# Kernel optimization log

Hardware: AMD Instinct MI355X
Metric: run time of the kernel (lower is better)

Reference implementation:

```python
import jax, jax.numpy as jnp
import numpy as np
import math

D_MODEL = 2048
NUM_HEADS = 16
D_FF = 8192
HEAD_DIM = D_MODEL // NUM_HEADS
EPS = 1e-5


def _xavier(key, out_f, in_f):
    std = math.sqrt(2.0 / (in_f + out_f))
    return jax.random.normal(key, (out_f, in_f), dtype=jnp.float32) * std


def setup_inputs() -> dict:
    key = jax.random.key(0)
    ks = jax.random.split(key, 8)
    x = jax.random.normal(ks[0], (2, 2048, D_MODEL), dtype=jnp.float32)
    return {
        "x": x,
        "Wq": _xavier(ks[1], D_MODEL, D_MODEL),
        "Wk": _xavier(ks[2], D_MODEL, D_MODEL),
        "Wv": _xavier(ks[3], D_MODEL, D_MODEL),
        "Wo": _xavier(ks[4], D_MODEL, D_MODEL),
        "W1": _xavier(ks[5], D_FF, D_MODEL),
        "W2": _xavier(ks[6], D_MODEL, D_FF),
        "g1": jnp.ones((D_MODEL,), jnp.float32),
        "b1": jnp.zeros((D_MODEL,), jnp.float32),
        "g2": jnp.ones((D_MODEL,), jnp.float32),
        "b2": jnp.zeros((D_MODEL,), jnp.float32),
    }


def _ternary(w):
    # per-tensor abs-mean threshold -> {-1, 0, 1}
    abs_w = jnp.abs(w)
    thr = jnp.mean(abs_w)
    return jnp.where(abs_w > thr, jnp.sign(w), jnp.zeros_like(w))


def _tlin(x, w):
    # F.linear with ternarized weight [out, in], no bias
    return jnp.einsum("bsi,oi->bso", x, _ternary(w))


def _layernorm(x, g, b):
    mu = jnp.mean(x, axis=-1, keepdims=True)
    var = jnp.mean(jnp.square(x - mu), axis=-1, keepdims=True)
    return (x - mu) * jax.lax.rsqrt(var + EPS) * g + b


def reference(x, Wq, Wk, Wv, Wo, W1, W2, g1, b1, g2, b2):
    B, S, D = x.shape
    H, Hd = NUM_HEADS, HEAD_DIM
    q = _tlin(x, Wq).reshape(B, S, H, Hd).transpose(0, 2, 1, 3)  # bhsd
    k = _tlin(x, Wk).reshape(B, S, H, Hd).transpose(0, 2, 1, 3)
    v = _tlin(x, Wv).reshape(B, S, H, Hd).transpose(0, 2, 1, 3)
    scores = jnp.einsum("bhqd,bhkd->bhqk", q, k) / math.sqrt(Hd)
    probs = jax.nn.softmax(scores, axis=-1)
    attn = jnp.einsum("bhqk,bhkd->bhqd", probs, v)
    attn = attn.transpose(0, 2, 1, 3).reshape(B, S, D)
    attn = _tlin(attn, Wo)
    x = _layernorm(x + attn, g1, b1)  # dropout is identity in eval
    ff = _tlin(jax.nn.relu(_tlin(x, W1)), W2)
    x = _layernorm(x + ff, g2, b2)
    return x
```

## Files before the change

### kernel.cpp

```cpp
#include <hip/hip_runtime.h>
#include <hip/hip_bf16.h>

typedef __bf16 bf16_t;
typedef __bf16 bf16x8 __attribute__((ext_vector_type(8)));
typedef __bf16 bf16x4 __attribute__((ext_vector_type(4)));
typedef float f32x4 __attribute__((ext_vector_type(4)));
typedef int i32x4 __attribute__((ext_vector_type(4)));

__device__ __forceinline__ f32x4 mfma16(bf16x8 a, bf16x8 b, f32x4 c) {
  return __builtin_amdgcn_mfma_f32_16x16x32_bf16(a, b, c, 0, 0, 0);
}

__device__ __forceinline__ void gload16(const void* g, void* l) {
  __builtin_amdgcn_global_load_lds(
      (const __attribute__((address_space(1))) void*)g,
      (__attribute__((address_space(3))) void*)l, 16, 0, 0);
}

__global__ void abssum_all(const float* __restrict__ W0, const float* __restrict__ W1_,
                           const float* __restrict__ W2_, const float* __restrict__ W3,
                           const float* __restrict__ W4, const float* __restrict__ W5,
                           double* __restrict__ partial) {
  __shared__ double sd[256];
  const int w = blockIdx.y, tid = threadIdx.x;
  const float* W = (w == 0) ? W0 : (w == 1) ? W1_ : (w == 2) ? W2_ : (w == 3) ? W3 : (w == 4) ? W4 : W5;
  const int n4 = (w < 4) ? 1048576 : 4194304;
  double s = 0.0;
  for (int i = blockIdx.x * 256 + tid; i < n4; i += 262144) {
    float4 v = ((const float4*)W)[i];
    s += (double)fabsf(v.x); s += (double)fabsf(v.y);
    s += (double)fabsf(v.z); s += (double)fabsf(v.w);
  }
  sd[tid] = s; __syncthreads();
  for (int st = 128; st > 0; st >>= 1) { if (tid < st) sd[tid] += sd[tid + st]; __syncthreads(); }
  if (tid == 0) partial[w * 1024 + blockIdx.x] = sd[0];
}

__global__ void abssum_fin(const double* __restrict__ partial, double* __restrict__ sums) {
  __shared__ double sd[256];
  const int tid = threadIdx.x;
  const double* p = partial + blockIdx.x * 1024;
  double s = p[tid] + p[tid + 256] + p[tid + 512] + p[tid + 768];
  sd[tid] = s; __syncthreads();
  for (int st = 128; st > 0; st >>= 1) { if (tid < st) sd[tid] += sd[tid + st]; __syncthreads(); }
  if (tid == 0) sums[blockIdx.x] = sd[0];
}

__global__ void ternarize4(const float* __restrict__ W0, const float* __restrict__ W1_,
                           const float* __restrict__ W2_, const float* __restrict__ W3,
                           bf16_t* __restrict__ out, const double* __restrict__ sums) {
  const int w = blockIdx.x >> 12;
  const float* W = (w == 0) ? W0 : (w == 1) ? W1_ : (w == 2) ? W2_ : W3;
  const double thr = sums[w] / 4194304.0;
  const int i = (blockIdx.x & 4095) * 256 + threadIdx.x;
  float4 v = ((const float4*)W)[i];
  bf16x4 o;
  float t;
  t = ((double)fabsf(v.x) > thr) ? (v.x > 0.f ? 1.f : -1.f) : 0.f; o[0] = (bf16_t)t;
  t = ((double)fabsf(v.y) > thr) ? (v.y > 0.f ? 1.f : -1.f) : 0.f; o[1] = (bf16_t)t;
  t = ((double)fabsf(v.z) > thr) ? (v.z > 0.f ? 1.f : -1.f) : 0.f; o[2] = (bf16_t)t;
  t = ((double)fabsf(v.w) > thr) ? (v.w > 0.f ? 1.f : -1.f) : 0.f; o[3] = (bf16_t)t;
  *(bf16x4*)&out[(size_t)w * 4194304 + (size_t)i * 4] = o;
}

__global__ void ternarize_k(const float* __restrict__ W, bf16_t* __restrict__ out,
                            const double* __restrict__ sum, double n) {
  const double thr = sum[0] / n;
  const int i = blockIdx.x * 256 + threadIdx.x;
  float4 v = ((const float4*)W)[i];
  bf16x4 o;
  float t;
  t = ((double)fabsf(v.x) > thr) ? (v.x > 0.f ? 1.f : -1.f) : 0.f; o[0] = (bf16_t)t;
  t = ((double)fabsf(v.y) > thr) ? (v.y > 0.f ? 1.f : -1.f) : 0.f; o[1] = (bf16_t)t;
  t = ((double)fabsf(v.z) > thr) ? (v.z > 0.f ? 1.f : -1.f) : 0.f; o[2] = (bf16_t)t;
  t = ((double)fabsf(v.w) > thr) ? (v.w > 0.f ? 1.f : -1.f) : 0.f; o[3] = (bf16_t)t;
  *(bf16x4*)&out[(size_t)i * 4] = o;
}

__global__ void split_x_k(const float* __restrict__ X, bf16_t* __restrict__ xhl) {
  const int i = blockIdx.x * 256 + threadIdx.x;
  const int t = i >> 9, col = (i & 511) * 4;
  float4 v = ((const float4*)X)[i];
  bf16x4 h, l;
  h[0] = (bf16_t)v.x; l[0] = (bf16_t)(v.x - (float)h[0]);
  h[1] = (bf16_t)v.y; l[1] = (bf16_t)(v.y - (float)h[1]);
  h[2] = (bf16_t)v.z; l[2] = (bf16_t)(v.z - (float)h[2]);
  h[3] = (bf16_t)v.w; l[3] = (bf16_t)(v.w - (float)h[3]);
  *(bf16x4*)&xhl[(size_t)t * 4096 + col] = h;
  *(bf16x4*)&xhl[(size_t)t * 4096 + 2048 + col] = l;
}

template <int EPI>
__global__ __launch_bounds__(512, 2) void gemmP(
    const bf16_t* __restrict__ Ah, const bf16_t* __restrict__ Bw,
    void* __restrict__ C0, int N, int K, int lda) {
  constexpr int BM = 128;
  __shared__ __align__(16) bf16_t sA[3][BM * 64];
  __shared__ __align__(16) bf16_t sB[3][256 * 64];

  const int tid = threadIdx.x;
  const int wid = tid >> 6, lane = tid & 63, lr = lane & 15, lg = lane >> 4;
  const int wr = wid >> 2, wc = wid & 3;
  const size_t Ks = (size_t)K;

  const int nwg = gridDim.x * gridDim.y;
  const int bid0 = blockIdx.y * gridDim.x + blockIdx.x;
  const int swz = (bid0 & 7) * (nwg >> 3) + (bid0 >> 3);
  const int bx = swz % gridDim.x, by = swz / gridDim.x;
  const size_t m0 = (size_t)by * BM, n0 = (size_t)bx * 256;
  const int nt = K / 64;

  f32x4 acc[4][4] = {};

  auto STAGEH = [&](int bi, int kt, int half) {
    const size_t ko = (size_t)kt * 64;
    if (half == 0) {
#pragma unroll
      for (int i = 0; i < 2; i++) {
        const int t = i * 512 + tid;
        const int r = t >> 3;
        const int su = (t & 7) ^ (r & 7);
        const int lo = (i * 512 + wid * 64) * 8;
        gload16(Ah + (m0 + r) * (size_t)lda + ko + su * 8, (void*)&sA[bi][lo]);
      }
      {
        const int r = tid >> 3;
        const int su = (tid & 7) ^ (r & 7);
        gload16(Bw + (n0 + r) * Ks + ko + su * 8, (void*)&sB[bi][(wid * 64) * 8]);
      }
    } else {
#pragma unroll
      for (int i = 1; i < 4; i++) {
        const int t = i * 512 + tid;
        const int r = t >> 3;
        const int su = (t & 7) ^ (r & 7);
        gload16(Bw + (n0 + r) * Ks + ko + su * 8, (void*)&sB[bi][(i * 512 + wid * 64) * 8]);
      }
    }
  };
  auto LDA = [&](const bf16_t* base, int m, int k) -> bf16x8 {
    const int row = wr * 64 + m * 16 + lr;
    const int u = (k * 4 + lg) ^ (lr & 7);
    return *(const bf16x8*)&base[row * 64 + u * 8];
  };
  auto LDB = [&](const bf16_t* base, int n, int k) -> bf16x8 {
    const int row = wc * 64 + n * 16 + lr;
    const int u = (k * 4 + lg) ^ (lr & 7);
    return *(const bf16x8*)&base[row * 64 + u * 8];
  };

  STAGEH(0, 0, 0); STAGEH(0, 0, 1);
  STAGEH(1, 1, 0); STAGEH(1, 1, 1);
  asm volatile("s_waitcnt vmcnt(6)" ::: "memory");
  __builtin_amdgcn_s_barrier();

  int bc = 0, bs = 2;
  for (int kt = 0; kt < nt; kt++) {
    const bool pf = (kt + 2 < nt);
    bf16x8 a[4][2], bfr[4][2];
#pragma unroll
    for (int m = 0; m < 4; m++)
#pragma unroll
      for (int k = 0; k < 2; k++) a[m][k] = LDA(&sA[bc][0], m, k);
#pragma unroll
    for (int n = 0; n < 2; n++)
#pragma unroll
      for (int k = 0; k < 2; k++) bfr[n][k] = LDB(&sB[bc][0], n, k);
    if (pf) STAGEH(bs, kt + 2, 0);
    __builtin_amdgcn_s_barrier();
    asm volatile("s_waitcnt lgkmcnt(0)" ::: "memory");
    __builtin_amdgcn_sched_barrier(0);
    __builtin_amdgcn_s_setprio(1);
#pragma unroll
    for (int k = 0; k < 2; k++)
#pragma unroll
      for (int m = 0; m < 4; m++)
#pragma unroll
        for (int n = 0; n < 2; n++) acc[m][n] = mfma16(a[m][k], bfr[n][k], acc[m][n]);
    __builtin_amdgcn_s_setprio(0);
    __builtin_amdgcn_s_barrier();
#pragma unroll
    for (int n = 0; n < 2; n++)
#pragma unroll
      for (int k = 0; k < 2; k++) bfr[n + 2][k] = LDB(&sB[bc][0], n + 2, k);
    if (pf) STAGEH(bs, kt + 2, 1);
    if (kt + 1 < nt) {
      if (pf) asm volatile("s_waitcnt vmcnt(6)" ::: "memory");
      else    asm volatile("s_waitcnt vmcnt(0)" ::: "memory");
    }
    __builtin_amdgcn_s_barrier();
    asm volatile("s_waitcnt lgkmcnt(0)" ::: "memory");
    __builtin_amdgcn_sched_barrier(0);
    __builtin_amdgcn_s_setprio(1);
#pragma unroll
    for (int k = 0; k < 2; k++)
#pragma unroll
      for (int m = 0; m < 4; m++)
#pragma unroll
        for (int n = 0; n < 2; n++) acc[m][n + 2] = mfma16(a[m][k], bfr[n + 2][k], acc[m][n + 2]);
    __builtin_amdgcn_s_setprio(0);
    __builtin_amdgcn_s_barrier();
    bc = (bc + 1 == 3) ? 0 : bc + 1;
    bs = (bs + 1 == 3) ? 0 : bs + 1;
  }

  const int row0 = (int)m0 + wr * 64, colb = (int)n0 + wc * 64;
#pragma unroll
  for (int m = 0; m < 4; m++)
#pragma unroll
    for (int n = 0; n < 4; n++)
#pragma unroll
      for (int j = 0; j < 4; j++) {
        const int r = row0 + m * 16 + lg * 4 + j;
        const int c = colb + n * 16 + lr;
        const float v = acc[m][n][j];
        if constexpr (EPI == 1) {
          const int bb = r >> 11, ss = r & 2047;
          ((bf16_t*)C0)[((size_t)bb * 2048 + c) * 2048 + ss] = (bf16_t)v;
        } else if constexpr (EPI == 2) {
          ((float*)C0)[(size_t)r * N + c] = v;
        } else {
          ((bf16_t*)C0)[(size_t)r * N + c] = (bf16_t)fmaxf(v, 0.f);
        }
      }
}

template <int EPI>
__global__ __launch_bounds__(512, 2) void gemm256(
    const bf16_t* __restrict__ A, const bf16_t* __restrict__ Bw,
    void* __restrict__ C0, void* __restrict__ C1,
    int N, int K, int lda, int ldb) {
  __shared__ __align__(16) bf16_t sA[2][256 * 64];
  __shared__ __align__(16) bf16_t sB[2][256 * 64];
  const int tid = threadIdx.x;
  const int wid = tid >> 6, lane = tid & 63, lr = lane & 15, lg = lane >> 4;
  const int wr = wid >> 2, wc = wid & 3;
  const int nwg = gridDim.x * gridDim.y;
  const int bid0 = blockIdx.y * gridDim.x + blockIdx.x;
  const int swz = (bid0 & 7) * (nwg >> 3) + (bid0 >> 3);
  const int bx = swz % gridDim.x, by = swz / gridDim.x;
  const size_t m0 = (size_t)by * 256, n0 = (size_t)bx * 256;
  const int nt = K / 64;
  const bf16_t* Abase = A + m0 * (size_t)lda;
  const bf16_t* Bbase = Bw + n0 * (size_t)ldb;

  f32x4 acc[8][4] = {};

  auto SG = [&](const bf16_t* base, bf16_t* dst, int kt, int h, int ld) {
    const size_t co = (size_t)((kt * 64) & (ld - 1));
#pragma unroll
    for (int i = 0; i < 2; i++) {
      const int e = (2 * h + i) * 512 + tid;
      const int r = e >> 3;
      const int su = (tid & 7) ^ (r & 7);
      gload16(base + (size_t)r * ld + co + su * 8,
              (void*)&dst[((2 * h + i) * 512 + wid * 64) * 8]);
    }
  };
  auto LDA = [&](int bi, int m, int k) -> bf16x8 {
    const int row = wr * 128 + m * 16 + lr;
    const int u = (k * 4 + lg) ^ (lr & 7);
    return *(const bf16x8*)&sA[bi][row * 64 + u * 8];
  };
  auto LDB = [&](int bi, int n, int k) -> bf16x8 {
    const int row = wc * 64 + n * 16 + lr;
    const int u = (k * 4 + lg) ^ (lr & 7);
    return *(const bf16x8*)&sB[bi][row * 64 + u * 8];
  };

  SG(Abase, sA[0], 0, 0, lda); SG(Abase, sA[0], 0, 1, lda);
  SG(Bbase, sB[0], 0, 0, ldb); SG(Bbase, sB[0], 0, 1, ldb);
  SG(Bbase, sB[1], 1, 0, ldb); SG(Bbase, sB[1], 1, 1, ldb); SG(Abase, sA[1], 1, 0, lda);
  asm volatile("s_waitcnt vmcnt(6)" ::: "memory");
  __builtin_amdgcn_s_barrier();

  for (int kt = 0; kt < nt; kt++) {
    const int bi = kt & 1, bn = bi ^ 1;
    bf16x8 a[4][2], b[4][2];
#pragma unroll
    for (int m = 0; m < 4; m++)
#pragma unroll
      for (int k = 0; k < 2; k++) a[m][k] = LDA(bi, m, k);
#pragma unroll
    for (int n = 0; n < 2; n++)
#pragma unroll
      for (int k = 0; k < 2; k++) b[n][k] = LDB(bi, n, k);
    if (kt + 1 < nt) SG(Abase, sA[bn], kt + 1, 1, lda);
    __builtin_amdgcn_s_barrier();
    asm volatile("s_waitcnt lgkmcnt(0)" ::: "memory");
    __builtin_amdgcn_sched_barrier(0);
    __builtin_amdgcn_s_setprio(1);
#pragma unroll
    for (int k = 0; k < 2; k++)
#pragma unroll
      for (int m = 0; m < 4; m++)
#pragma unroll
        for (int n = 0; n < 2; n++) acc[m][n] = mfma16(a[m][k], b[n][k], acc[m][n]);
    __builtin_amdgcn_s_setprio(0);
    __builtin_amdgcn_s_barrier();
#pragma unroll
    for (int n = 0; n < 2; n++)
#pragma unroll
      for (int k = 0; k < 2; k++) b[n + 2][k] = LDB(bi, n + 2, k);
    if (kt + 2 < nt) SG(Bbase, sB[bi], kt + 2, 0, ldb);
    __builtin_amdgcn_s_barrier();
    asm volatile("s_waitcnt lgkmcnt(0)" ::: "memory");
    __builtin_amdgcn_sched_barrier(0);
    __builtin_amdgcn_s_setprio(1);
#pragma unroll
    for (int k = 0; k < 2; k++)
#pragma unroll
      for (int m = 0; m < 4; m++)
#pragma unroll
        for (int n = 0; n < 2; n++) acc[m][n + 2] = mfma16(a[m][k], b[n + 2][k], acc[m][n + 2]);
    __builtin_amdgcn_s_setprio(0);
    __builtin_amdgcn_s_barrier();
#pragma unroll
    for (int m = 0; m < 4; m++)
#pragma unroll
      for (int k = 0; k < 2; k++) a[m][k] = LDA(bi, m + 4, k);
    if (kt + 2 < nt) SG(Bbase, sB[bi], kt + 2, 1, ldb);
    __builtin_amdgcn_s_barrier();
    asm volatile("s_waitcnt lgkmcnt(0)" ::: "memory");
    __builtin_amdgcn_sched_barrier(0);
    __builtin_amdgcn_s_setprio(1);
#pragma unroll
    for (int k = 0; k < 2; k++)
#pragma unroll
      for (int m = 0; m < 4; m++)
#pragma unroll
        for (int n = 0; n < 2; n++) acc[m + 4][n + 2] = mfma16(a[m][k], b[n + 2][k], acc[m + 4][n + 2]);
    __builtin_amdgcn_s_setprio(0);
    __builtin_amdgcn_s_barrier();
    if (kt + 2 < nt) SG(Abase, sA[bi], kt + 2, 0, lda);
    __builtin_amdgcn_s_setprio(1);
#pragma unroll
    for (int k = 0; k < 2; k++)
#pragma unroll
      for (int m = 0; m < 4; m++)
#pragma unroll
        for (int n = 0; n < 2; n++) acc[m + 4][n] = mfma16(a[m][k], b[n][k], acc[m + 4][n]);
    __builtin_amdgcn_s_setprio(0);
    if (kt + 1 < nt) {
      if (kt + 2 < nt) asm volatile("s_waitcnt vmcnt(6)" ::: "memory");
      else             asm volatile("s_waitcnt vmcnt(0)" ::: "memory");
    }
    __builtin_amdgcn_s_barrier();
  }

  const int row0 = (int)m0 + wr * 128, colb = (int)n0 + wc * 64;
#pragma unroll
  for (int m = 0; m < 8; m++)
#pragma unroll
    for (int n = 0; n < 4; n++)
#pragma unroll
      for (int j = 0; j < 4; j++) {
        const int r = row0 + m * 16 + lg * 4 + j;
        const int c = colb + n * 16 + lr;
        const float v = acc[m][n][j];
        if constexpr (EPI == 0) {
          bf16_t hi = (bf16_t)v;
          ((bf16_t*)C0)[(size_t)r * N + c] = hi;
          ((bf16_t*)C1)[(size_t)r * N + c] = (bf16_t)(v - (float)hi);
        } else {
          ((bf16_t*)C0)[(size_t)r * N + c] = (bf16_t)fmaxf(v, 0.f);
        }
      }
}

__global__ __launch_bounds__(256, 2) void attn_k(
    const bf16_t* __restrict__ qh, const bf16_t* __restrict__ ql,
    const bf16_t* __restrict__ kh, const bf16_t* __restrict__ kl,
    const bf16_t* __restrict__ vT, bf16_t* __restrict__ out) {
  __shared__ __align__(16) bf16_t sKh[2 * 8192];
  __shared__ __align__(16) bf16_t sKl[2 * 8192];
  __shared__ __align__(16) bf16_t plds[4][2048];

  const int fid = blockIdx.y * 16 + blockIdx.x;
  const int qt = fid >> 5;
  const int bh = (fid & 7) * 4 + ((fid >> 3) & 3);
  const int b = bh >> 4, h = bh & 15;
  const int wv = threadIdx.x >> 6, lane = threadIdx.x & 63, lr = lane & 15, lg = lane >> 4;
  const size_t tok0 = (size_t)b * 2048 + qt * 128 + wv * 16;
  bf16_t* pw = &plds[wv][0];

  auto STAGE = [&](int bufi, int kv0n) {
#pragma unroll
    for (int i = 0; i < 4; i++) {
      const int tt = wv * 4 + i;
      const int r = tt * 4 + (lane >> 4);
      const int ce = ((lane & 15) ^ (r & 7)) * 8;
      const size_t gofs = ((size_t)b * 2048 + kv0n + r) * 4096 + h * 128 + ce;
      gload16(kh + gofs, (void*)&sKh[bufi * 8192 + tt * 512]);
      gload16(kl + gofs, (void*)&sKl[bufi * 8192 + tt * 512]);
    }
  };

  bf16x8 qhf[2][4], qlf[2][4];
#pragma unroll
  for (int t = 0; t < 2; t++) {
    const bf16_t* qp = qh + (tok0 + t * 64 + lr) * 4096 + h * 128 + lg * 8;
    const bf16_t* qp2 = ql + (tok0 + t * 64 + lr) * 4096 + h * 128 + lg * 8;
#pragma unroll
    for (int ks = 0; ks < 4; ks++) {
      qhf[t][ks] = *(const bf16x8*)(qp + ks * 32);
      qlf[t][ks] = *(const bf16x8*)(qp2 + ks * 32);
    }
  }
  f32x4 oacc[2][8] = {};
  float mrun[2] = {-1e30f, -1e30f};
  float lrun[2] = {0.f, 0.f};
  const bf16_t* vbase = vT + ((size_t)b * 2048 + h * 128) * 2048;
  const float sc = 0.08838834764831845f;
  const int swz8 = 2 * (lr & 7);

  STAGE(0, 0);
  for (int c = 0; c < 32; c++) {
    const int kv0 = c * 64;
    if (c + 1 < 32) {
      STAGE((c + 1) & 1, kv0 + 64);
      asm volatile("s_waitcnt vmcnt(8)" ::: "memory");
    } else {
      asm volatile("s_waitcnt vmcnt(0)" ::: "memory");
    }
    __builtin_amdgcn_s_barrier();

    const int bufo = (c & 1) * 8192;
    f32x4 s[2][4] = {};
    __builtin_amdgcn_s_setprio(1);
#pragma unroll
    for (int nb = 0; nb < 4; nb++) {
      const int rbase = bufo + (nb * 16 + lr) * 128;
#pragma unroll
      for (int ks = 0; ks < 4; ks++) {
        const int u = (((ks * 4 + lg) ^ (lr & 7)) * 8);
        bf16x8 kf = *(const bf16x8*)&sKh[rbase + u];
        bf16x8 kg = *(const bf16x8*)&sKl[rbase + u];
        s[0][nb] = mfma16(kf, qhf[0][ks], s[0][nb]);
        s[1][nb] = mfma16(kf, qhf[1][ks], s[1][nb]);
        s[0][nb] = mfma16(kf, qlf[0][ks], s[0][nb]);
        s[1][nb] = mfma16(kf, qlf[1][ks], s[1][nb]);
        s[0][nb] = mfma16(kg, qhf[0][ks], s[0][nb]);
        s[1][nb] = mfma16(kg, qhf[1][ks], s[1][nb]);
      }
    }
    __builtin_amdgcn_s_setprio(0);

    float resc[2];
    bool skip[2];
#pragma unroll
    for (int t = 0; t < 2; t++) {
#pragma unroll
      for (int nb = 0; nb < 4; nb++) s[t][nb] *= sc;
      f32x4 m4 = __builtin_elementwise_max(
          __builtin_elementwise_max(s[t][0], s[t][1]),
          __builtin_elementwise_max(s[t][2], s[t][3]));
      float mx = fmaxf(fmaxf(m4[0], m4[1]), fmaxf(m4[2], m4[3]));
      mx = fmaxf(mx, __shfl_xor(mx, 16));
      mx = fmaxf(mx, __shfl_xor(mx, 32));
      skip[t] = (__all(mx <= mrun[t] + 8.f) != 0);
      float rs_ = 1.f;
      if (!skip[t]) {
        const float mnew = fmaxf(mrun[t], mx);
        rs_ = __expf(mrun[t] - mnew);
        mrun[t] = mnew;
      }
      resc[t] = rs_;
      float ls = 0.f;
#pragma unroll
      for (int nb = 0; nb < 4; nb++) {
        bf16x4 pk;
#pragma unroll
        for (int j = 0; j < 4; j++) {
          const float p = __expf(s[t][nb][j] - mrun[t]);
          ls += p;
          pk[j] = (bf16_t)p;
        }
        const int s8 = (4 * nb + lg) ^ swz8;
        *(bf16x4*)&pw[t * 1024 + lr * 64 + s8 * 4] = pk;
      }
      ls += __shfl_xor(ls, 16);
      ls += __shfl_xor(ls, 32);
      lrun[t] = lrun[t] * rs_ + ls;
    }
    asm volatile("s_waitcnt lgkmcnt(0)" ::: "memory");
    __builtin_amdgcn_sched_barrier(0);
    bf16x8 pfr[2][2];
#pragma unroll
    for (int t = 0; t < 2; t++)
#pragma unroll
      for (int kc = 0; kc < 2; kc++) {
        const int se = (8 * kc + 2 * lg) ^ swz8;
        pfr[t][kc] = *(const bf16x8*)&pw[t * 1024 + lr * 64 + se * 4];
      }
    if (!skip[0]) {
#pragma unroll
      for (int dt = 0; dt < 8; dt++) oacc[0][dt] *= resc[0];
    }
    if (!skip[1]) {
#pragma unroll
      for (int dt = 0; dt < 8; dt++) oacc[1][dt] *= resc[1];
    }

    const bf16_t* vp = vbase + kv0 + lg * 8;
    __builtin_amdgcn_s_setprio(1);
#pragma unroll
    for (int dt = 0; dt < 8; dt++) {
      const bf16_t* vr = vp + (size_t)(dt * 16 + lr) * 2048;
      bf16x8 v0 = *(const bf16x8*)(vr);
      bf16x8 v1 = *(const bf16x8*)(vr + 32);
      oacc[0][dt] = mfma16(v0, pfr[0][0], oacc[0][dt]);
      oacc[1][dt] = mfma16(v0, pfr[1][0], oacc[1][dt]);
      oacc[0][dt] = mfma16(v1, pfr[0][1], oacc[0][dt]);
      oacc[1][dt] = mfma16(v1, pfr[1][1], oacc[1][dt]);
    }
    __builtin_amdgcn_s_setprio(0);
    asm volatile("" ::: "memory");
    __builtin_amdgcn_s_barrier();
  }

  {
    bf16_t* ep = &sKh[wv * 2176];
    const int q = lane >> 2, c4 = lane & 3;
    const int qs = 2 * (q & 7);
#pragma unroll
    for (int t = 0; t < 2; t++) {
      const float inv = 1.f / lrun[t];
#pragma unroll
      for (int dt = 0; dt < 8; dt++) {
        bf16x4 pk;
#pragma unroll
        for (int j = 0; j < 4; j++) pk[j] = (bf16_t)(oacc[t][dt][j] * inv);
        const int s5 = (4 * dt + lg) ^ swz8;
        *(bf16x4*)&ep[lr * 136 + s5 * 4] = pk;
      }
      asm volatile("s_waitcnt lgkmcnt(0)" ::: "memory");
      __builtin_amdgcn_sched_barrier(0);
      bf16_t* orow = out + (tok0 + t * 64 + q) * 2048 + h * 128 + c4 * 32;
#pragma unroll
      for (int i = 0; i < 4; i++) {
        const int se = (c4 * 8 + 2 * i) ^ qs;
        bf16x8 vv = *(const bf16x8*)&ep[q * 136 + se * 4];
        *(bf16x8*)(orow + i * 8) = vv;
      }
      asm volatile("s_waitcnt lgkmcnt(0)" ::: "memory");
    }
  }
}

__global__ __launch_bounds__(256) void ln_k(
    const float* __restrict__ X, const float* __restrict__ R,
    const float* __restrict__ G, const float* __restrict__ Bt,
    float* __restrict__ O32, bf16_t* __restrict__ O16) {
  const int t = blockIdx.x, tid = threadIdx.x;
  const float4* xp = (const float4*)(X + (size_t)t * 2048);
  const float4* rp = (const float4*)(R + (size_t)t * 2048);
  float4 v0 = xp[tid], w0 = rp[tid];
  float4 v1 = xp[tid + 256], w1 = rp[tid + 256];
  v0.x += w0.x; v0.y += w0.y; v0.z += w0.z; v0.w += w0.w;
  v1.x += w1.x; v1.y += w1.y; v1.z += w1.z; v1.w += w1.w;
  float sum = v0.x + v0.y + v0.z + v0.w + v1.x + v1.y + v1.z + v1.w;
  float sq = v0.x * v0.x + v0.y * v0.y + v0.z * v0.z + v0.w * v0.w +
             v1.x * v1.x + v1.y * v1.y + v1.z * v1.z + v1.w * v1.w;
  for (int d = 1; d < 64; d <<= 1) { sum += __shfl_xor(sum, d); sq += __shfl_xor(sq, d); }
  __shared__ float s1[4], s2[4];
  const int wv = tid >> 6, lane = tid & 63;
  if (lane == 0) { s1[wv] = sum; s2[wv] = sq; }
  __syncthreads();
  const float tot = s1[0] + s1[1] + s1[2] + s1[3];
  const float tsq = s2[0] + s2[1] + s2[2] + s2[3];
  const float mu = tot * (1.f / 2048.f);
  const float var = tsq * (1.f / 2048.f) - mu * mu;
  const float rs = 1.f / sqrtf(var + 1e-5f);
  const float4* gp = (const float4*)G;
  const float4* bp = (const float4*)Bt;
  float4 g0 = gp[tid], g1v = gp[tid + 256], b0 = bp[tid], b1v = bp[tid + 256];
  float4 o0, o1;
  o0.x = (v0.x - mu) * rs * g0.x + b0.x; o0.y = (v0.y - mu) * rs * g0.y + b0.y;
  o0.z = (v0.z - mu) * rs * g0.z + b0.z; o0.w = (v0.w - mu) * rs * g0.w + b0.w;
  o1.x = (v1.x - mu) * rs * g1v.x + b1v.x; o1.y = (v1.y - mu) * rs * g1v.y + b1v.y;
  o1.z = (v1.z - mu) * rs * g1v.z + b1v.z; o1.w = (v1.w - mu) * rs * g1v.w + b1v.w;
  ((float4*)(O32 + (size_t)t * 2048))[tid] = o0;
  ((float4*)(O32 + (size_t)t * 2048))[tid + 256] = o1;
  if (O16) {
    bf16x4 h0, h1;
    h0[0] = (bf16_t)o0.x; h0[1] = (bf16_t)o0.y; h0[2] = (bf16_t)o0.z; h0[3] = (bf16_t)o0.w;
    h1[0] = (bf16_t)o1.x; h1[1] = (bf16_t)o1.y; h1[2] = (bf16_t)o1.z; h1[3] = (bf16_t)o1.w;
    *(bf16x4*)&O16[(size_t)t * 2048 + tid * 4] = h0;
    *(bf16x4*)&O16[(size_t)t * 2048 + 1024 + tid * 4] = h1;
  }
}

extern "C" void kernel_launch(void* const* d_in, const int* in_sizes, int n_in,
                              void* d_out, int out_size, void* d_ws, size_t ws_size,
                              hipStream_t stream) {
  const float* x  = (const float*)d_in[0];
  const float* Wq = (const float*)d_in[1];
  const float* Wk = (const float*)d_in[2];
  const float* Wv = (const float*)d_in[3];
  const float* Wo = (const float*)d_in[4];
  const float* W1 = (const float*)d_in[5];
  const float* W2 = (const float*)d_in[6];
  const float* g1 = (const float*)d_in[7];
  const float* b1 = (const float*)d_in[8];
  const float* g2 = (const float*)d_in[9];
  const float* b2 = (const float*)d_in[10];
  float* out = (float*)d_out;
  char* ws = (char*)d_ws;

  constexpr size_t SZB = (size_t)4096 * 2048 * 2;
  bf16_t* xhl = (bf16_t*)(ws + 0 * SZB);
  bf16_t* qkh = (bf16_t*)(ws + 2 * SZB);
  bf16_t* qkl = (bf16_t*)(ws + 4 * SZB);
  bf16_t* vt  = (bf16_t*)(ws + 6 * SZB);
  bf16_t* at  = (bf16_t*)(ws + 7 * SZB);
  float* o32  = (float*)(ws + 8 * SZB);
  bf16_t* wt  = (bf16_t*)(ws + 8 * SZB + (size_t)4096 * 2048 * 4);
  double* red = (double*)(ws + 8 * SZB + (size_t)4096 * 2048 * 4 + (size_t)8192 * 2048 * 2);
  double* sums = red + 8192;
  float* h1 = (float*)ws;
  bf16_t* h1b = qkh;
  bf16_t* f1 = (bf16_t*)(ws + 4 * SZB);
  float* g32 = o32;
  (void)in_sizes; (void)n_in; (void)out_size; (void)ws_size;

  abssum_all<<<dim3(1024, 6), 256, 0, stream>>>(Wq, Wk, Wv, Wo, W1, W2, red);
  abssum_fin<<<6, 256, 0, stream>>>(red, sums);
  split_x_k<<<8192, 256, 0, stream>>>(x, xhl);
  ternarize4<<<16384, 256, 0, stream>>>(Wq, Wk, Wv, Wo, wt, sums);

  gemm256<0><<<dim3(16, 16), 512, 0, stream>>>(xhl, wt, qkh, qkl, 4096, 4096, 4096, 2048);
  gemmP<1><<<dim3(8, 32), 512, 0, stream>>>(xhl, wt + 8388608, vt, 2048, 2048, 4096);
  attn_k<<<dim3(16, 32), 256, 0, stream>>>(qkh, qkl, qkh + 2048, qkl + 2048, vt, at);
  gemmP<2><<<dim3(8, 32), 512, 0, stream>>>(at, wt + 12582912, o32, 2048, 2048, 2048);
  ln_k<<<4096, 256, 0, stream>>>(x, o32, g1, b1, h1, h1b);
  ternarize_k<<<16384, 256, 0, stream>>>(W1, wt, sums + 4, 16777216.0);
  gemm256<3><<<dim3(32, 16), 512, 0, stream>>>(h1b, wt, f1, nullptr, 8192, 2048, 2048, 2048);
  ternarize_k<<<16384, 256, 0, stream>>>(W2, wt, sums + 5, 16777216.0);
  gemmP<2><<<dim3(8, 32), 512, 0, stream>>>(f1, wt, g32, 2048, 8192, 8192);
  ln_k<<<4096, 256, 0, stream>>>(h1, g32, g2, b2, out, nullptr);
}
```

Measured before the change: 795.2 us.

## Split-K the W2 GEMM on the 256 tile, fuse the partial sums into the final LayerNorm

New measurement: 851.9 us. 1.07x slower.

```diff
diff --git a/kernel.cpp b/kernel.cpp
--- a/kernel.cpp
+++ b/kernel.cpp
@@ -217,15 +217,13 @@
         if constexpr (EPI == 1) {
           const int bb = r >> 11, ss = r & 2047;
           ((bf16_t*)C0)[((size_t)bb * 2048 + c) * 2048 + ss] = (bf16_t)v;
-        } else if constexpr (EPI == 2) {
+        } else {
           ((float*)C0)[(size_t)r * N + c] = v;
-        } else {
-          ((bf16_t*)C0)[(size_t)r * N + c] = (bf16_t)fmaxf(v, 0.f);
         }
       }
 }
 
-template <int EPI>
+template <int EPI, int MB>
 __global__ __launch_bounds__(512, 2) void gemm256(
     const bf16_t* __restrict__ A, const bf16_t* __restrict__ Bw,
     void* __restrict__ C0, void* __restrict__ C1,
@@ -239,7 +237,9 @@
   const int bid0 = blockIdx.y * gridDim.x + blockIdx.x;
   const int swz = (bid0 & 7) * (nwg >> 3) + (bid0 >> 3);
   const int bx = swz % gridDim.x, by = swz / gridDim.x;
-  const size_t m0 = (size_t)by * 256, n0 = (size_t)bx * 256;
+  const int mt = by & ((1 << MB) - 1), kh = by >> MB;
+  const int koff = kh * K;
+  const size_t m0 = (size_t)mt * 256, n0 = (size_t)bx * 256;
   const int nt = K / 64;
   const bf16_t* Abase = A + m0 * (size_t)lda;
   const bf16_t* Bbase = Bw + n0 * (size_t)ldb;
@@ -247,7 +247,7 @@
   f32x4 acc[8][4] = {};
 
   auto SG = [&](const bf16_t* base, bf16_t* dst, int kt, int h, int ld) {
-    const size_t co = (size_t)((kt * 64) & (ld - 1));
+    const size_t co = (size_t)((kt * 64 + koff) & (ld - 1));
 #pragma unroll
     for (int i = 0; i < 2; i++) {
       const int e = (2 * h + i) * 512 + tid;
@@ -362,6 +362,9 @@
           bf16_t hi = (bf16_t)v;
           ((bf16_t*)C0)[(size_t)r * N + c] = hi;
           ((bf16_t*)C1)[(size_t)r * N + c] = (bf16_t)(v - (float)hi);
+        } else if constexpr (EPI == 4) {
+          float* dst = (float*)(kh ? C1 : C0);
+          dst[(size_t)r * N + c] = v;
         } else {
           ((bf16_t*)C0)[(size_t)r * N + c] = (bf16_t)fmaxf(v, 0.f);
         }
@@ -373,7 +376,6 @@
     const bf16_t* __restrict__ kh, const bf16_t* __restrict__ kl,
     const bf16_t* __restrict__ vT, bf16_t* __restrict__ out) {
   __shared__ __align__(16) bf16_t sKh[2 * 8192];
-  __shared__ __align__(16) bf16_t sKl[2 * 8192];
   __shared__ __align__(16) bf16_t plds[4][2048];
 
   const int fid = blockIdx.y * 16 + blockIdx.x;
@@ -392,7 +394,6 @@
       const int ce = ((lane & 15) ^ (r & 7)) * 8;
       const size_t gofs = ((size_t)b * 2048 + kv0n + r) * 4096 + h * 128 + ce;
       gload16(kh + gofs, (void*)&sKh[bufi * 8192 + tt * 512]);
-      gload16(kl + gofs, (void*)&sKl[bufi * 8192 + tt * 512]);
     }
   };
 
@@ -419,7 +420,7 @@
     const int kv0 = c * 64;
     if (c + 1 < 32) {
       STAGE((c + 1) & 1, kv0 + 64);
-      asm volatile("s_waitcnt vmcnt(8)" ::: "memory");
+      asm volatile("s_waitcnt vmcnt(4)" ::: "memory");
     } else {
       asm volatile("s_waitcnt vmcnt(0)" ::: "memory");
     }
@@ -431,11 +432,12 @@
 #pragma unroll
     for (int nb = 0; nb < 4; nb++) {
       const int rbase = bufo + (nb * 16 + lr) * 128;
+      const bf16_t* klrow = kl + ((size_t)b * 2048 + kv0 + nb * 16 + lr) * 4096 + h * 128 + lg * 8;
 #pragma unroll
       for (int ks = 0; ks < 4; ks++) {
         const int u = (((ks * 4 + lg) ^ (lr & 7)) * 8);
         bf16x8 kf = *(const bf16x8*)&sKh[rbase + u];
-        bf16x8 kg = *(const bf16x8*)&sKl[rbase + u];
+        bf16x8 kg = *(const bf16x8*)(klrow + ks * 32);
         s[0][nb] = mfma16(kf, qhf[0][ks], s[0][nb]);
         s[1][nb] = mfma16(kf, qhf[1][ks], s[1][nb]);
         s[0][nb] = mfma16(kf, qlf[0][ks], s[0][nb]);
@@ -580,8 +582,10 @@
   o0.z = (v0.z - mu) * rs * g0.z + b0.z; o0.w = (v0.w - mu) * rs * g0.w + b0.w;
   o1.x = (v1.x - mu) * rs * g1v.x + b1v.x; o1.y = (v1.y - mu) * rs * g1v.y + b1v.y;
   o1.z = (v1.z - mu) * rs * g1v.z + b1v.z; o1.w = (v1.w - mu) * rs * g1v.w + b1v.w;
-  ((float4*)(O32 + (size_t)t * 2048))[tid] = o0;
-  ((float4*)(O32 + (size_t)t * 2048))[tid + 256] = o1;
+  if (O32) {
+    ((float4*)(O32 + (size_t)t * 2048))[tid] = o0;
+    ((float4*)(O32 + (size_t)t * 2048))[tid + 256] = o1;
+  }
   if (O16) {
     bf16x4 h0, h1;
     h0[0] = (bf16_t)o0.x; h0[1] = (bf16_t)o0.y; h0[2] = (bf16_t)o0.z; h0[3] = (bf16_t)o0.w;
@@ -589,6 +593,46 @@
     *(bf16x4*)&O16[(size_t)t * 2048 + tid * 4] = h0;
     *(bf16x4*)&O16[(size_t)t * 2048 + 1024 + tid * 4] = h1;
   }
+}
+
+__global__ __launch_bounds__(256) void ln2_k(
+    const bf16_t* __restrict__ Xb, const float* __restrict__ R0, const float* __restrict__ R1,
+    const float* __restrict__ G, const float* __restrict__ Bt, float* __restrict__ out) {
+  const int t = blockIdx.x, tid = threadIdx.x;
+  bf16x4 x0 = *(const bf16x4*)&Xb[(size_t)t * 2048 + tid * 4];
+  bf16x4 x1 = *(const bf16x4*)&Xb[(size_t)t * 2048 + 1024 + tid * 4];
+  const float4* r0p = (const float4*)(R0 + (size_t)t * 2048);
+  const float4* r1p = (const float4*)(R1 + (size_t)t * 2048);
+  float4 a0 = r0p[tid], a1 = r0p[tid + 256];
+  float4 c0 = r1p[tid], c1 = r1p[tid + 256];
+  float4 v0, v1;
+  v0.x = (float)x0[0] + a0.x + c0.x; v0.y = (float)x0[1] + a0.y + c0.y;
+  v0.z = (float)x0[2] + a0.z + c0.z; v0.w = (float)x0[3] + a0.w + c0.w;
+  v1.x = (float)x1[0] + a1.x + c1.x; v1.y = (float)x1[1] + a1.y + c1.y;
+  v1.z = (float)x1[2] + a1.z + c1.z; v1.w = (float)x1[3] + a1.w + c1.w;
+  float sum = v0.x + v0.y + v0.z + v0.w + v1.x + v1.y + v1.z + v1.w;
+  float sq = v0.x * v0.x + v0.y * v0.y + v0.z * v0.z + v0.w * v0.w +
+             v1.x * v1.x + v1.y * v1.y + v1.z * v1.z + v1.w * v1.w;
+  for (int d = 1; d < 64; d <<= 1) { sum += __shfl_xor(sum, d); sq += __shfl_xor(sq, d); }
+  __shared__ float s1[4], s2[4];
+  const int wv = tid >> 6, lane = tid & 63;
+  if (lane == 0) { s1[wv] = sum; s2[wv] = sq; }
+  __syncthreads();
+  const float tot = s1[0] + s1[1] + s1[2] + s1[3];
+  const float tsq = s2[0] + s2[1] + s2[2] + s2[3];
+  const float mu = tot * (1.f / 2048.f);
+  const float var = tsq * (1.f / 2048.f) - mu * mu;
+  const float rs = 1.f / sqrtf(var + 1e-5f);
+  const float4* gp = (const float4*)G;
+  const float4* bp = (const float4*)Bt;
+  float4 g0 = gp[tid], g1v = gp[tid + 256], b0 = bp[tid], b1v = bp[tid + 256];
+  float4 o0, o1;
+  o0.x = (v0.x - mu) * rs * g0.x + b0.x; o0.y = (v0.y - mu) * rs * g0.y + b0.y;
+  o0.z = (v0.z - mu) * rs * g0.z + b0.z; o0.w = (v0.w - mu) * rs * g0.w + b0.w;
+  o1.x = (v1.x - mu) * rs * g1v.x + b1v.x; o1.y = (v1.y - mu) * rs * g1v.y + b1v.y;
+  o1.z = (v1.z - mu) * rs * g1v.z + b1v.z; o1.w = (v1.w - mu) * rs * g1v.w + b1v.w;
+  ((float4*)(out + (size_t)t * 2048))[tid] = o0;
+  ((float4*)(out + (size_t)t * 2048))[tid + 256] = o1;
 }
 
 extern "C" void kernel_launch(void* const* d_in, const int* in_sizes, int n_in,
@@ -618,10 +662,10 @@
   bf16_t* wt  = (bf16_t*)(ws + 8 * SZB + (size_t)4096 * 2048 * 4);
   double* red = (double*)(ws + 8 * SZB + (size_t)4096 * 2048 * 4 + (size_t)8192 * 2048 * 2);
   double* sums = red + 8192;
-  float* h1 = (float*)ws;
   bf16_t* h1b = qkh;
   bf16_t* f1 = (bf16_t*)(ws + 4 * SZB);
-  float* g32 = o32;
+  float* g32a = o32;
+  float* g32b = (float*)(ws + 0 * SZB);
   (void)in_sizes; (void)n_in; (void)out_size; (void)ws_size;
 
   abssum_all<<<dim3(1024, 6), 256, 0, stream>>>(Wq, Wk, Wv, Wo, W1, W2, red);
@@ -629,14 +673,14 @@
   split_x_k<<<8192, 256, 0, stream>>>(x, xhl);
   ternarize4<<<16384, 256, 0, stream>>>(Wq, Wk, Wv, Wo, wt, sums);
 
-  gemm256<0><<<dim3(16, 16), 512, 0, stream>>>(xhl, wt, qkh, qkl, 4096, 4096, 4096, 2048);
+  gemm256<0, 8><<<dim3(16, 16), 512, 0, stream>>>(xhl, wt, qkh, qkl, 4096, 4096, 4096, 2048);
   gemmP<1><<<dim3(8, 32), 512, 0, stream>>>(xhl, wt + 8388608, vt, 2048, 2048, 4096);
   attn_k<<<dim3(16, 32), 256, 0, stream>>>(qkh, qkl, qkh + 2048, qkl + 2048, vt, at);
   gemmP<2><<<dim3(8, 32), 512, 0, stream>>>(at, wt + 12582912, o32, 2048, 2048, 2048);
-  ln_k<<<4096, 256, 0, stream>>>(x, o32, g1, b1, h1, h1b);
+  ln_k<<<4096, 256, 0, stream>>>(x, o32, g1, b1, nullptr, h1b);
   ternarize_k<<<16384, 256, 0, stream>>>(W1, wt, sums + 4, 16777216.0);
-  gemm256<3><<<dim3(32, 16), 512, 0, stream>>>(h1b, wt, f1, nullptr, 8192, 2048, 2048, 2048);
+  gemm256<3, 8><<<dim3(32, 16), 512, 0, stream>>>(h1b, wt, f1, nullptr, 8192, 2048, 2048, 2048);
   ternarize_k<<<16384, 256, 0, stream>>>(W2, wt, sums + 5, 16777216.0);
-  gemmP<2><<<dim3(8, 32), 512, 0, stream>>>(f1, wt, g32, 2048, 8192, 8192);
-  ln_k<<<4096, 256, 0, stream>>>(h1, g32, g2, b2, out, nullptr);
-}
+  gemm256<4, 4><<<dim3(8, 32), 512, 0, stream>>>(f1, wt, g32a, g32b, 2048, 4096, 8192, 8192);
+  ln2_k<<<4096, 256, 0, stream>>>(h1b, g32a, g32b, g2, b2, out);
+}
```
